# Kernel optimization log

Measured on AMD Instinct MI355X. Metric: run time of the kernel, lower is better.

## Reference

```python
import jax, jax.numpy as jnp
import numpy as np

N_TOKENS = 4096
N_EMBD = 1024
N_EXPERTS = 8
TOP_K = 2
TEMPERATURE = 1.0
PARAM_SCALE = 0.02


def setup_inputs() -> dict:
    key = jax.random.key(0)
    ks = jax.random.split(key, 6)
    x = jax.random.normal(ks[0], (N_TOKENS, N_EMBD), dtype=jnp.float32)
    gate_w = jax.random.normal(ks[1], (N_EMBD, N_EXPERTS), dtype=jnp.float32) * PARAM_SCALE
    w1 = jax.random.normal(ks[2], (N_EXPERTS, N_EMBD, 4 * N_EMBD), dtype=jnp.float32) * PARAM_SCALE
    b1 = jax.random.normal(ks[3], (N_EXPERTS, 4 * N_EMBD), dtype=jnp.float32) * PARAM_SCALE
    w2 = jax.random.normal(ks[4], (N_EXPERTS, 4 * N_EMBD, N_EMBD), dtype=jnp.float32) * PARAM_SCALE
    b2 = jax.random.normal(ks[5], (N_EXPERTS, N_EMBD), dtype=jnp.float32) * PARAM_SCALE
    return {"x": x, "gate_w": gate_w, "w1": w1, "b1": b1, "w2": w2, "b2": b2}


def reference(x, gate_w, w1, b1, w2, b2):
    # Gating: softmax with temperature, top-2, renormalize over the top-2.
    gate_logits = x @ gate_w                              # [N, E]
    gate_probs = jax.nn.softmax(gate_logits / TEMPERATURE, axis=-1)
    top_v, top_i = jax.lax.top_k(gate_probs, TOP_K)       # [N, k]
    top_v = top_v / jnp.sum(top_v, axis=-1, keepdims=True)
    # Per-expert combine weight: sum of renormalized top-k probs routed to e.
    one_hot = jax.nn.one_hot(top_i, N_EXPERTS, dtype=x.dtype)   # [N, k, E]
    combine = jnp.einsum('nk,nke->ne', top_v, one_hot)          # [N, E]
    # Dense expert evaluation (faithful math; loop over fixed small expert set).
    out = jnp.zeros_like(x)
    for e in range(N_EXPERTS):
        h = jax.nn.gelu(x @ w1[e] + b1[e], approximate=False)   # [N, 4C]
        y = h @ w2[e] + b2[e]                                   # [N, C]
        out = out + combine[:, e:e + 1] * y
    return out
```

## Files before the change

### kernel.cpp

```cpp
#include <hip/hip_runtime.h>
#include <math.h>

#define TOKENS 4096
#define EMBD   1024
#define HID    4096
#define NE     8
#define SLOTC  8320

typedef __attribute__((ext_vector_type(8))) short short8;
typedef __attribute__((ext_vector_type(4))) float f32x4;

#define GLOBAL_PTR(p) ((const __attribute__((address_space(1))) void*)(p))
#define LDS_PTR(p)    ((__attribute__((address_space(3))) void*)(p))

#define SWZ(row, q) ((row) * 32 + (((q) ^ (((row) >> 1) & 3)) * 8))

__device__ __forceinline__ unsigned short f2bf(float f) {
  unsigned int u = __float_as_uint(f);
  u += 0x7FFFu + ((u >> 16) & 1u);
  return (unsigned short)(u >> 16);
}
__device__ __forceinline__ float bf2f(unsigned short h) {
  return __uint_as_float((unsigned int)h << 16);
}

__device__ __forceinline__ float fast_gelu(float v) {
  float u = fabsf(v) * 0.70710678118654752f;
  float t = 1.0f / (1.0f + 0.3275911f * u);
  float poly = ((((1.061405429f * t - 1.453152027f) * t + 1.421413741f) * t
                 - 0.284496736f) * t + 0.254829592f) * t;
  float erf_abs = 1.0f - poly * __expf(-u * u);
  float er = (v < 0.0f) ? -erf_abs : erf_abs;
  return 0.5f * v * (1.0f + er);
}

__global__ __launch_bounds__(256) void k_gate_cvt(const float* __restrict__ x,
                                                  const float* __restrict__ gw,
                                                  unsigned short* __restrict__ xb,
                                                  int* __restrict__ idx2,
                                                  float* __restrict__ wv) {
  int wave = threadIdx.x >> 6, lane = threadIdx.x & 63;
  int t = blockIdx.x * 4 + wave;
  const float4* xr = (const float4*)(x + (size_t)t * EMBD);
  ushort4* xbr = (ushort4*)(xb + (size_t)t * EMBD);
  float acc[NE];
#pragma unroll
  for (int e = 0; e < NE; e++) acc[e] = 0.f;
#pragma unroll
  for (int ch = 0; ch < 4; ch++) {
    int i = ch * 64 + lane;
    float4 v = xr[i];
    ushort4 o;
    o.x = f2bf(v.x); o.y = f2bf(v.y); o.z = f2bf(v.z); o.w = f2bf(v.w);
    xbr[i] = o;
    int c = i * 4;
    const float* g0 = gw + (size_t)c * NE;
#pragma unroll
    for (int e = 0; e < NE; e++) acc[e] += v.x * g0[e];
#pragma unroll
    for (int e = 0; e < NE; e++) acc[e] += v.y * g0[NE + e];
#pragma unroll
    for (int e = 0; e < NE; e++) acc[e] += v.z * g0[2 * NE + e];
#pragma unroll
    for (int e = 0; e < NE; e++) acc[e] += v.w * g0[3 * NE + e];
  }
#pragma unroll
  for (int e = 0; e < NE; e++) {
#pragma unroll
    for (int off = 32; off > 0; off >>= 1) acc[e] += __shfl_down(acc[e], off);
  }
  if (lane == 0) {
    float best = -1e30f, second = -1e30f;
    int bi = 0, si = 0;
#pragma unroll
    for (int e = 0; e < NE; e++) {
      float l = acc[e];
      if (l > best) { second = best; si = bi; best = l; bi = e; }
      else if (l > second) { second = l; si = e; }
    }
    float b = expf(second - best);
    float w0 = 1.f / (1.f + b);
    float w1 = b / (1.f + b);
    idx2[2 * t] = bi; idx2[2 * t + 1] = si;
    wv[2 * t] = w0; wv[2 * t + 1] = w1;
  }
}

__global__ __launch_bounds__(256) void k_count(const int* __restrict__ idx2,
                                               int* __restrict__ ctrl) {
  __shared__ int cnt[NE];
  int tid = threadIdx.x;
  if (tid < NE) cnt[tid] = 0;
  __syncthreads();
  for (int i = tid; i < TOKENS * 2; i += 256) atomicAdd(&cnt[idx2[i]], 1);
  __syncthreads();
  if (tid == 0) {
    int off = 0;
#pragma unroll
    for (int e = 0; e < NE; e++) { int c = cnt[e]; ctrl[e] = c; ctrl[8 + e] = off; off += c; }
    ctrl[16] = off;
  }
  if (tid < NE) ctrl[17 + tid] = 0;
}

__global__ __launch_bounds__(256) void k_assign(const int* __restrict__ idx2,
                                                int* __restrict__ ctrl,
                                                int* __restrict__ token_list,
                                                int* __restrict__ tok2slot) {
  __shared__ int lpos[NE];
  __shared__ int lbase[NE];
  int tid = threadIdx.x;
  int t = blockIdx.x * 256 + tid;
  if (tid < NE) lpos[tid] = 0;
  __syncthreads();
  int e0 = idx2[2 * t], e1 = idx2[2 * t + 1];
  int p0 = atomicAdd(&lpos[e0], 1);
  int p1 = atomicAdd(&lpos[e1], 1);
  __syncthreads();
  if (tid < NE) lbase[tid] = atomicAdd(&ctrl[17 + tid], lpos[tid]);
  __syncthreads();
  int s0 = ctrl[8 + e0] + lbase[e0] + p0;
  int s1 = ctrl[8 + e1] + lbase[e1] + p1;
  token_list[s0] = t;
  token_list[s1] = t;
  tok2slot[2 * t] = s0;
  tok2slot[2 * t + 1] = s1;
}

__global__ __launch_bounds__(256) void k_trans(const float* __restrict__ in,
                                               unsigned short* __restrict__ out,
                                               int R, int C) {
  __shared__ unsigned short T[64 * 66];
  int e = blockIdx.z;
  const float* ine = in + (size_t)e * R * C;
  unsigned short* oute = out + (size_t)e * R * C;
  int r0 = blockIdx.y * 64;
  int c0 = blockIdx.x * 64;
  int tid = threadIdx.x;
  {
    int c4 = tid & 15;
    int rb = tid >> 4;
#pragma unroll
    for (int it = 0; it < 4; it++) {
      int r = rb + 16 * it;
      float4 v = *(const float4*)(ine + (size_t)(r0 + r) * C + c0 + 4 * c4);
      T[(4 * c4 + 0) * 66 + r] = f2bf(v.x);
      T[(4 * c4 + 1) * 66 + r] = f2bf(v.y);
      T[(4 * c4 + 2) * 66 + r] = f2bf(v.z);
      T[(4 * c4 + 3) * 66 + r] = f2bf(v.w);
    }
  }
  __syncthreads();
  {
    int rr = tid & 7;
    int cq = tid >> 3;
#pragma unroll
    for (int it = 0; it < 2; it++) {
      int c = cq + 32 * it;
      short8 o;
#pragma unroll
      for (int k = 0; k < 8; k++) o[k] = (short)T[c * 66 + 8 * rr + k];
      *(short8*)(oute + (size_t)(c0 + c) * R + r0 + 8 * rr) = o;
    }
  }
}

__global__ __launch_bounds__(256, 2) void k_gemm1(
    const unsigned short* __restrict__ xb,
    const unsigned short* __restrict__ w1t,
    const float* __restrict__ b1,
    const int* __restrict__ ctrl,
    const int* __restrict__ token_list,
    unsigned short* __restrict__ Hbuf) {
  int h = blockIdx.x;
  int e = h & 7;
  int j = h >> 3;
  int nb = (j & 31) * 128;
  int m_base = (j >> 5) * 128;
  int cnt = ctrl[e];
  if (m_base >= cnt) return;
  int off_e = ctrl[8 + e];
  int tid = threadIdx.x;
  int wave = tid >> 6, lane = tid & 63;

  __shared__ __align__(16) unsigned short As[2][128 * 32];
  __shared__ __align__(16) unsigned short Bs[2][128 * 32];

  int chS = (tid & 3) ^ ((tid >> 3) & 3);
  int rowA0 = tid >> 2;
  int rowA1 = 64 + (tid >> 2);
  int tok0 = token_list[off_e + min(m_base + rowA0, cnt - 1)];
  int tok1 = token_list[off_e + min(m_base + rowA1, cnt - 1)];
  const unsigned short* srcA0 = xb + (size_t)tok0 * EMBD + chS * 8;
  const unsigned short* srcA1 = xb + (size_t)tok1 * EMBD + chS * 8;
  const unsigned short* wb = w1t + (size_t)e * HID * EMBD;
  const unsigned short* srcB0 = wb + (size_t)(nb + rowA0) * EMBD + chS * 8;
  const unsigned short* srcB1 = wb + (size_t)(nb + rowA1) * EMBD + chS * 8;

  f32x4 acc[4][4];
#pragma unroll
  for (int i = 0; i < 4; i++)
#pragma unroll
    for (int j2 = 0; j2 < 4; j2++) acc[i][j2] = (f32x4){0.f, 0.f, 0.f, 0.f};

  int wm = (wave >> 1) * 64, wn = (wave & 1) * 64;
  int q4 = lane >> 4, cc = lane & 15;

#define STAGE1(buf, k0) do {                                                                            \
    __builtin_amdgcn_global_load_lds(GLOBAL_PTR(srcA0 + (k0)), LDS_PTR((char*)&As[buf][0] + wave * 1024), 16, 0, 0);        \
    __builtin_amdgcn_global_load_lds(GLOBAL_PTR(srcA1 + (k0)), LDS_PTR((char*)&As[buf][0] + 4096 + wave * 1024), 16, 0, 0); \
    __builtin_amdgcn_global_load_lds(GLOBAL_PTR(srcB0 + (k0)), LDS_PTR((char*)&Bs[buf][0] + wave * 1024), 16, 0, 0);        \
    __builtin_amdgcn_global_load_lds(GLOBAL_PTR(srcB1 + (k0)), LDS_PTR((char*)&Bs[buf][0] + 4096 + wave * 1024), 16, 0, 0); \
  } while (0)

#define COMPUTE1(buf) do {                                                                   \
    short8 af[4], bfr[4];                                                                    \
    _Pragma("unroll")                                                                        \
    for (int i = 0; i < 4; i++) af[i] = *(const short8*)(&As[buf][0] + SWZ(wm + i * 16 + cc, q4));   \
    _Pragma("unroll")                                                                        \
    for (int j2 = 0; j2 < 4; j2++) bfr[j2] = *(const short8*)(&Bs[buf][0] + SWZ(wn + j2 * 16 + cc, q4)); \
    _Pragma("unroll")                                                                        \
    for (int i = 0; i < 4; i++)                                                              \
      _Pragma("unroll")                                                                      \
      for (int j2 = 0; j2 < 4; j2++)                                                         \
        acc[i][j2] = __builtin_amdgcn_mfma_f32_16x16x32_bf16(af[i], bfr[j2], acc[i][j2], 0, 0, 0); \
  } while (0)

  STAGE1(0, 0);
  __syncthreads();
  int cur = 0;
  for (int k0 = 32; k0 < EMBD; k0 += 32) {
    STAGE1(cur ^ 1, k0);
    __builtin_amdgcn_sched_barrier(0);
    COMPUTE1(cur);
    __syncthreads();
    cur ^= 1;
  }
  COMPUTE1(cur);

  const float* b1e = b1 + (size_t)e * HID;
  float bias[4];
#pragma unroll
  for (int j2 = 0; j2 < 4; j2++) bias[j2] = b1e[nb + wn + j2 * 16 + cc];
#pragma unroll
  for (int i = 0; i < 4; i++) {
#pragma unroll
    for (int r = 0; r < 4; r++) {
      int m_loc = wm + i * 16 + q4 * 4 + r;
      int m = m_base + m_loc;
      if (m < cnt) {
        size_t hrow = (size_t)(off_e + m) * HID;
#pragma unroll
        for (int j2 = 0; j2 < 4; j2++)
          Hbuf[hrow + nb + wn + j2 * 16 + cc] = f2bf(fast_gelu(acc[i][j2][r] + bias[j2]));
      }
    }
  }
#undef STAGE1
#undef COMPUTE1
}

__global__ __launch_bounds__(256, 2) void k_gemm2(
    const unsigned short* __restrict__ Hbuf,
    const unsigned short* __restrict__ w2t,
    const int* __restrict__ ctrl,
    unsigned short* __restrict__ Yp) {
  int h = blockIdx.x;
  int e = h & 7;
  int s = (h >> 3) & 1;
  int rem = h >> 4;
  int m_base = (rem >> 3) * 128;
  int nb = (rem & 7) * 128;
  int cnt = ctrl[e];
  if (m_base >= cnt) return;
  int off_e = ctrl[8 + e];
  int tid = threadIdx.x;
  int wave = tid >> 6, lane = tid & 63;

  __shared__ __align__(16) unsigned short As[2][128 * 32];
  __shared__ __align__(16) unsigned short Bs[2][128 * 32];

  int chS = (tid & 3) ^ ((tid >> 3) & 3);
  int rowA0 = tid >> 2;
  int rowA1 = 64 + (tid >> 2);
  const unsigned short* srcA0 = Hbuf + (size_t)(off_e + m_base + rowA0) * HID + chS * 8;
  const unsigned short* srcA1 = Hbuf + (size_t)(off_e + m_base + rowA1) * HID + chS * 8;
  const unsigned short* wb = w2t + (size_t)e * EMBD * HID;
  const unsigned short* srcB0 = wb + (size_t)(nb + rowA0) * HID + chS * 8;
  const unsigned short* srcB1 = wb + (size_t)(nb + rowA1) * HID + chS * 8;

  f32x4 acc[4][4];
#pragma unroll
  for (int i = 0; i < 4; i++)
#pragma unroll
    for (int j2 = 0; j2 < 4; j2++) acc[i][j2] = (f32x4){0.f, 0.f, 0.f, 0.f};

  int wm = (wave >> 1) * 64, wn = (wave & 1) * 64;
  int q4 = lane >> 4, cc = lane & 15;

#define STAGE2(buf, k0) do {                                                                            \
    __builtin_amdgcn_global_load_lds(GLOBAL_PTR(srcA0 + (k0)), LDS_PTR((char*)&As[buf][0] + wave * 1024), 16, 0, 0);        \
    __builtin_amdgcn_global_load_lds(GLOBAL_PTR(srcA1 + (k0)), LDS_PTR((char*)&As[buf][0] + 4096 + wave * 1024), 16, 0, 0); \
    __builtin_amdgcn_global_load_lds(GLOBAL_PTR(srcB0 + (k0)), LDS_PTR((char*)&Bs[buf][0] + wave * 1024), 16, 0, 0);        \
    __builtin_amdgcn_global_load_lds(GLOBAL_PTR(srcB1 + (k0)), LDS_PTR((char*)&Bs[buf][0] + 4096 + wave * 1024), 16, 0, 0); \
  } while (0)

#define COMPUTE2(buf) do {                                                                   \
    short8 af[4], bfr[4];                                                                    \
    _Pragma("unroll")                                                                        \
    for (int i = 0; i < 4; i++) af[i] = *(const short8*)(&As[buf][0] + SWZ(wm + i * 16 + cc, q4));   \
    _Pragma("unroll")                                                                        \
    for (int j2 = 0; j2 < 4; j2++) bfr[j2] = *(const short8*)(&Bs[buf][0] + SWZ(wn + j2 * 16 + cc, q4)); \
    _Pragma("unroll")                                                                        \
    for (int i = 0; i < 4; i++)                                                              \
      _Pragma("unroll")                                                                      \
      for (int j2 = 0; j2 < 4; j2++)                                                         \
        acc[i][j2] = __builtin_amdgcn_mfma_f32_16x16x32_bf16(af[i], bfr[j2], acc[i][j2], 0, 0, 0); \
  } while (0)

  int kbeg = s * (HID / 2), kend = kbeg + HID / 2;
  STAGE2(0, kbeg);
  __syncthreads();
  int cur = 0;
  for (int k0 = kbeg + 32; k0 < kend; k0 += 32) {
    STAGE2(cur ^ 1, k0);
    __builtin_amdgcn_sched_barrier(0);
    COMPUTE2(cur);
    __syncthreads();
    cur ^= 1;
  }
  COMPUTE2(cur);

  unsigned short* Yps = Yp + (size_t)s * SLOTC * EMBD;
#pragma unroll
  for (int i = 0; i < 4; i++) {
#pragma unroll
    for (int r = 0; r < 4; r++) {
      int m_loc = wm + i * 16 + q4 * 4 + r;
      int m = m_base + m_loc;
      if (m < cnt) {
        size_t yrow = (size_t)(off_e + m) * EMBD;
#pragma unroll
        for (int j2 = 0; j2 < 4; j2++)
          Yps[yrow + nb + wn + j2 * 16 + cc] = f2bf(acc[i][j2][r]);
      }
    }
  }
#undef STAGE2
#undef COMPUTE2
}

__global__ __launch_bounds__(256) void k_combine(const unsigned short* __restrict__ Yp,
                                                 const float* __restrict__ b2,
                                                 const int* __restrict__ idx2,
                                                 const float* __restrict__ wv,
                                                 const int* __restrict__ tok2slot,
                                                 float* __restrict__ out) {
  int t = blockIdx.x;
  int tid = threadIdx.x;
  int c = tid * 4;
  int e0 = idx2[2 * t], e1 = idx2[2 * t + 1];
  float w0 = wv[2 * t], w1 = wv[2 * t + 1];
  int s0 = tok2slot[2 * t], s1 = tok2slot[2 * t + 1];
  ushort4 p00 = *(const ushort4*)(Yp + ((size_t)0 * SLOTC + s0) * EMBD + c);
  ushort4 p01 = *(const ushort4*)(Yp + ((size_t)1 * SLOTC + s0) * EMBD + c);
  ushort4 p10 = *(const ushort4*)(Yp + ((size_t)0 * SLOTC + s1) * EMBD + c);
  ushort4 p11 = *(const ushort4*)(Yp + ((size_t)1 * SLOTC + s1) * EMBD + c);
  float4 b20 = *(const float4*)(b2 + (size_t)e0 * EMBD + c);
  float4 b21 = *(const float4*)(b2 + (size_t)e1 * EMBD + c);
  float4 r;
  r.x = w0 * (bf2f(p00.x) + bf2f(p01.x) + b20.x) + w1 * (bf2f(p10.x) + bf2f(p11.x) + b21.x);
  r.y = w0 * (bf2f(p00.y) + bf2f(p01.y) + b20.y) + w1 * (bf2f(p10.y) + bf2f(p11.y) + b21.y);
  r.z = w0 * (bf2f(p00.z) + bf2f(p01.z) + b20.z) + w1 * (bf2f(p10.z) + bf2f(p11.z) + b21.z);
  r.w = w0 * (bf2f(p00.w) + bf2f(p01.w) + b20.w) + w1 * (bf2f(p10.w) + bf2f(p11.w) + b21.w);
  *(float4*)(out + (size_t)t * EMBD + c) = r;
}

extern "C" void kernel_launch(void* const* d_in, const int* in_sizes, int n_in,
                              void* d_out, int out_size, void* d_ws, size_t ws_size,
                              hipStream_t stream) {
  (void)in_sizes; (void)n_in; (void)out_size; (void)ws_size;
  const float* x      = (const float*)d_in[0];
  const float* gate_w = (const float*)d_in[1];
  const float* w1     = (const float*)d_in[2];
  const float* b1     = (const float*)d_in[3];
  const float* w2     = (const float*)d_in[4];
  const float* b2     = (const float*)d_in[5];
  float* out = (float*)d_out;

  char* ws = (char*)d_ws;
  size_t off = 0;
  auto alloc = [&](size_t bytes) {
    char* p = ws + off;
    off += (bytes + 255) & ~(size_t)255;
    return p;
  };
  unsigned short* xb    = (unsigned short*)alloc((size_t)TOKENS * EMBD * 2);
  unsigned short* w1t   = (unsigned short*)alloc((size_t)NE * HID * EMBD * 2);
  unsigned short* w2t   = (unsigned short*)alloc((size_t)NE * EMBD * HID * 2);
  unsigned short* Hbuf  = (unsigned short*)alloc((size_t)SLOTC * HID * 2);
  unsigned short* Yp    = (unsigned short*)alloc((size_t)2 * SLOTC * EMBD * 2);
  int*   token_list     = (int*)alloc((size_t)SLOTC * 4);
  int*   idx2           = (int*)alloc((size_t)TOKENS * 2 * 4);
  float* wv             = (float*)alloc((size_t)TOKENS * 2 * 4);
  int*   tok2slot       = (int*)alloc((size_t)TOKENS * 2 * 4);
  int*   ctrl           = (int*)alloc(32 * 4);

  k_gate_cvt<<<TOKENS / 4, 256, 0, stream>>>(x, gate_w, xb, idx2, wv);
  k_count<<<1, 256, 0, stream>>>(idx2, ctrl);
  k_assign<<<TOKENS / 256, 256, 0, stream>>>(idx2, ctrl, token_list, tok2slot);
  k_trans<<<dim3(HID / 64, EMBD / 64, NE), 256, 0, stream>>>(w1, w1t, EMBD, HID);
  k_trans<<<dim3(EMBD / 64, HID / 64, NE), 256, 0, stream>>>(w2, w2t, HID, EMBD);
  k_gemm1<<<8192, 256, 0, stream>>>(xb, w1t, b1, ctrl, token_list, Hbuf);
  k_gemm2<<<4096, 256, 0, stream>>>(Hbuf, w2t, ctrl, Yp);
  k_combine<<<TOKENS, 256, 0, stream>>>(Yp, b2, idx2, wv, tok2slot, out);
}
```

Baseline: 561.4 us.

## Use 256x256 tiles with 8 waves and 4-stage LDS pipeline in expert GEMMs

```diff
diff --git a/kernel.cpp b/kernel.cpp
--- a/kernel.cpp
+++ b/kernel.cpp
@@ -12,8 +12,6 @@
 
 #define GLOBAL_PTR(p) ((const __attribute__((address_space(1))) void*)(p))
 #define LDS_PTR(p)    ((__attribute__((address_space(3))) void*)(p))
-
-#define SWZ(row, q) ((row) * 32 + (((q) ^ (((row) >> 1) & 3)) * 8))
 
 __device__ __forceinline__ unsigned short f2bf(float f) {
   unsigned int u = __float_as_uint(f);
@@ -165,7 +163,32 @@
   }
 }
 
-__global__ __launch_bounds__(256, 2) void k_gemm1(
+
+#define STAGE_G(sA0_, sA1_, sB0_, sB1_, kk, sl) do {                                              \
+    __builtin_amdgcn_global_load_lds(GLOBAL_PTR((sA0_) + (kk)), LDS_PTR(lds + (sl) * 16384 + wave * 2048), 16, 0, 0);          \
+    __builtin_amdgcn_global_load_lds(GLOBAL_PTR((sA1_) + (kk)), LDS_PTR(lds + (sl) * 16384 + wave * 2048 + 1024), 16, 0, 0);   \
+    __builtin_amdgcn_global_load_lds(GLOBAL_PTR((sB0_) + (kk)), LDS_PTR(lds + 65536 + (sl) * 16384 + wave * 2048), 16, 0, 0);  \
+    __builtin_amdgcn_global_load_lds(GLOBAL_PTR((sB1_) + (kk)), LDS_PTR(lds + 65536 + (sl) * 16384 + wave * 2048 + 1024), 16, 0, 0); \
+  } while (0)
+
+#define STEP_BODY(sl) do {                                                                        \
+    const short8* Ap = (const short8*)(lds + (sl) * 16384 + aoff);                                \
+    const short8* Bp = (const short8*)(lds + 65536 + (sl) * 16384 + boff);                        \
+    short8 af[8], bfr[4];                                                                         \
+    _Pragma("unroll")                                                                             \
+    for (int f = 0; f < 8; f++) af[f] = Ap[f * 64];                                               \
+    _Pragma("unroll")                                                                             \
+    for (int n = 0; n < 4; n++) bfr[n] = Bp[n * 64];                                              \
+    __builtin_amdgcn_s_setprio(1);                                                                \
+    _Pragma("unroll")                                                                             \
+    for (int f = 0; f < 8; f++)                                                                   \
+      _Pragma("unroll")                                                                           \
+      for (int n = 0; n < 4; n++)                                                                 \
+        acc[f][n] = __builtin_amdgcn_mfma_f32_16x16x32_bf16(af[f], bfr[n], acc[f][n], 0, 0, 0);   \
+    __builtin_amdgcn_s_setprio(0);                                                                \
+  } while (0)
+
+__global__ __launch_bounds__(512, 2) void k_gemm1(
     const unsigned short* __restrict__ xb,
     const unsigned short* __restrict__ w1t,
     const float* __restrict__ b1,
@@ -175,92 +198,75 @@
   int h = blockIdx.x;
   int e = h & 7;
   int j = h >> 3;
-  int nb = (j & 31) * 128;
-  int m_base = (j >> 5) * 128;
+  int m_base = (j & 15) * 256;
+  int nb = (j >> 4) * 256;
   int cnt = ctrl[e];
   if (m_base >= cnt) return;
   int off_e = ctrl[8 + e];
   int tid = threadIdx.x;
   int wave = tid >> 6, lane = tid & 63;
-
-  __shared__ __align__(16) unsigned short As[2][128 * 32];
-  __shared__ __align__(16) unsigned short Bs[2][128 * 32];
-
-  int chS = (tid & 3) ^ ((tid >> 3) & 3);
-  int rowA0 = tid >> 2;
-  int rowA1 = 64 + (tid >> 2);
-  int tok0 = token_list[off_e + min(m_base + rowA0, cnt - 1)];
-  int tok1 = token_list[off_e + min(m_base + rowA1, cnt - 1)];
-  const unsigned short* srcA0 = xb + (size_t)tok0 * EMBD + chS * 8;
-  const unsigned short* srcA1 = xb + (size_t)tok1 * EMBD + chS * 8;
-  const unsigned short* wb = w1t + (size_t)e * HID * EMBD;
-  const unsigned short* srcB0 = wb + (size_t)(nb + rowA0) * EMBD + chS * 8;
-  const unsigned short* srcB1 = wb + (size_t)(nb + rowA1) * EMBD + chS * 8;
-
-  f32x4 acc[4][4];
-#pragma unroll
-  for (int i = 0; i < 4; i++)
-#pragma unroll
-    for (int j2 = 0; j2 < 4; j2++) acc[i][j2] = (f32x4){0.f, 0.f, 0.f, 0.f};
-
-  int wm = (wave >> 1) * 64, wn = (wave & 1) * 64;
+  int wr = wave >> 2, wc = wave & 3;
   int q4 = lane >> 4, cc = lane & 15;
 
-#define STAGE1(buf, k0) do {                                                                            \
-    __builtin_amdgcn_global_load_lds(GLOBAL_PTR(srcA0 + (k0)), LDS_PTR((char*)&As[buf][0] + wave * 1024), 16, 0, 0);        \
-    __builtin_amdgcn_global_load_lds(GLOBAL_PTR(srcA1 + (k0)), LDS_PTR((char*)&As[buf][0] + 4096 + wave * 1024), 16, 0, 0); \
-    __builtin_amdgcn_global_load_lds(GLOBAL_PTR(srcB0 + (k0)), LDS_PTR((char*)&Bs[buf][0] + wave * 1024), 16, 0, 0);        \
-    __builtin_amdgcn_global_load_lds(GLOBAL_PTR(srcB1 + (k0)), LDS_PTR((char*)&Bs[buf][0] + 4096 + wave * 1024), 16, 0, 0); \
-  } while (0)
-
-#define COMPUTE1(buf) do {                                                                   \
-    short8 af[4], bfr[4];                                                                    \
-    _Pragma("unroll")                                                                        \
-    for (int i = 0; i < 4; i++) af[i] = *(const short8*)(&As[buf][0] + SWZ(wm + i * 16 + cc, q4));   \
-    _Pragma("unroll")                                                                        \
-    for (int j2 = 0; j2 < 4; j2++) bfr[j2] = *(const short8*)(&Bs[buf][0] + SWZ(wn + j2 * 16 + cc, q4)); \
-    _Pragma("unroll")                                                                        \
-    for (int i = 0; i < 4; i++)                                                              \
-      _Pragma("unroll")                                                                      \
-      for (int j2 = 0; j2 < 4; j2++)                                                         \
-        acc[i][j2] = __builtin_amdgcn_mfma_f32_16x16x32_bf16(af[i], bfr[j2], acc[i][j2], 0, 0, 0); \
-  } while (0)
-
-  STAGE1(0, 0);
-  __syncthreads();
-  int cur = 0;
-  for (int k0 = 32; k0 < EMBD; k0 += 32) {
-    STAGE1(cur ^ 1, k0);
+  __shared__ __align__(16) char lds[131072];
+
+  int qg = (lane & 3) ^ ((lane >> 3) & 3);
+  int row0 = wave * 32 + (lane >> 2);
+  int row1 = row0 + 16;
+  int tok0 = token_list[off_e + min(m_base + row0, cnt - 1)];
+  int tok1 = token_list[off_e + min(m_base + row1, cnt - 1)];
+  const unsigned short* sA0 = xb + (size_t)tok0 * EMBD + qg * 8;
+  const unsigned short* sA1 = xb + (size_t)tok1 * EMBD + qg * 8;
+  const unsigned short* wbp = w1t + (size_t)e * HID * EMBD;
+  const unsigned short* sB0 = wbp + (size_t)(nb + row0) * EMBD + qg * 8;
+  const unsigned short* sB1 = wbp + (size_t)(nb + row1) * EMBD + qg * 8;
+
+  int swz = (q4 ^ ((cc >> 1) & 3)) * 16;
+  int aoff = (wr * 128 + cc) * 64 + swz;
+  int boff = (wc * 64 + cc) * 64 + swz;
+
+  f32x4 acc[8][4];
+#pragma unroll
+  for (int f = 0; f < 8; f++)
+#pragma unroll
+    for (int n = 0; n < 4; n++) acc[f][n] = (f32x4){0.f, 0.f, 0.f, 0.f};
+
+  STAGE_G(sA0, sA1, sB0, sB1, 0, 0);
+  STAGE_G(sA0, sA1, sB0, sB1, 32, 1);
+  STAGE_G(sA0, sA1, sB0, sB1, 64, 2);
+
+#pragma unroll 4
+  for (int c = 0; c < 32; ++c) {
+    asm volatile("s_waitcnt vmcnt(8)" ::: "memory");
+    __builtin_amdgcn_s_barrier();
     __builtin_amdgcn_sched_barrier(0);
-    COMPUTE1(cur);
-    __syncthreads();
-    cur ^= 1;
-  }
-  COMPUTE1(cur);
+    int kk = ((c + 3) * 32) & (EMBD - 1);
+    STAGE_G(sA0, sA1, sB0, sB1, kk, (c + 3) & 3);
+    STEP_BODY(c & 3);
+  }
+  asm volatile("s_waitcnt vmcnt(0)" ::: "memory");
 
   const float* b1e = b1 + (size_t)e * HID;
   float bias[4];
 #pragma unroll
-  for (int j2 = 0; j2 < 4; j2++) bias[j2] = b1e[nb + wn + j2 * 16 + cc];
-#pragma unroll
-  for (int i = 0; i < 4; i++) {
+  for (int n = 0; n < 4; n++) bias[n] = b1e[nb + wc * 64 + n * 16 + cc];
+#pragma unroll
+  for (int f = 0; f < 8; f++) {
 #pragma unroll
     for (int r = 0; r < 4; r++) {
-      int m_loc = wm + i * 16 + q4 * 4 + r;
+      int m_loc = wr * 128 + f * 16 + q4 * 4 + r;
       int m = m_base + m_loc;
       if (m < cnt) {
         size_t hrow = (size_t)(off_e + m) * HID;
 #pragma unroll
-        for (int j2 = 0; j2 < 4; j2++)
-          Hbuf[hrow + nb + wn + j2 * 16 + cc] = f2bf(fast_gelu(acc[i][j2][r] + bias[j2]));
+        for (int n = 0; n < 4; n++)
+          Hbuf[hrow + nb + wc * 64 + n * 16 + cc] = f2bf(fast_gelu(acc[f][n][r] + bias[n]));
       }
     }
   }
-#undef STAGE1
-#undef COMPUTE1
-}
-
-__global__ __launch_bounds__(256, 2) void k_gemm2(
+}
+
+__global__ __launch_bounds__(512, 2) void k_gemm2(
     const unsigned short* __restrict__ Hbuf,
     const unsigned short* __restrict__ w2t,
     const int* __restrict__ ctrl,
@@ -268,86 +274,71 @@
   int h = blockIdx.x;
   int e = h & 7;
   int s = (h >> 3) & 1;
-  int rem = h >> 4;
-  int m_base = (rem >> 3) * 128;
-  int nb = (rem & 7) * 128;
+  int j = h >> 4;
+  int m_base = (j & 15) * 256;
+  int nb = (j >> 4) * 256;
   int cnt = ctrl[e];
   if (m_base >= cnt) return;
   int off_e = ctrl[8 + e];
   int tid = threadIdx.x;
   int wave = tid >> 6, lane = tid & 63;
-
-  __shared__ __align__(16) unsigned short As[2][128 * 32];
-  __shared__ __align__(16) unsigned short Bs[2][128 * 32];
-
-  int chS = (tid & 3) ^ ((tid >> 3) & 3);
-  int rowA0 = tid >> 2;
-  int rowA1 = 64 + (tid >> 2);
-  const unsigned short* srcA0 = Hbuf + (size_t)(off_e + m_base + rowA0) * HID + chS * 8;
-  const unsigned short* srcA1 = Hbuf + (size_t)(off_e + m_base + rowA1) * HID + chS * 8;
-  const unsigned short* wb = w2t + (size_t)e * EMBD * HID;
-  const unsigned short* srcB0 = wb + (size_t)(nb + rowA0) * HID + chS * 8;
-  const unsigned short* srcB1 = wb + (size_t)(nb + rowA1) * HID + chS * 8;
-
-  f32x4 acc[4][4];
-#pragma unroll
-  for (int i = 0; i < 4; i++)
-#pragma unroll
-    for (int j2 = 0; j2 < 4; j2++) acc[i][j2] = (f32x4){0.f, 0.f, 0.f, 0.f};
-
-  int wm = (wave >> 1) * 64, wn = (wave & 1) * 64;
+  int wr = wave >> 2, wc = wave & 3;
   int q4 = lane >> 4, cc = lane & 15;
 
-#define STAGE2(buf, k0) do {                                                                            \
-    __builtin_amdgcn_global_load_lds(GLOBAL_PTR(srcA0 + (k0)), LDS_PTR((char*)&As[buf][0] + wave * 1024), 16, 0, 0);        \
-    __builtin_amdgcn_global_load_lds(GLOBAL_PTR(srcA1 + (k0)), LDS_PTR((char*)&As[buf][0] + 4096 + wave * 1024), 16, 0, 0); \
-    __builtin_amdgcn_global_load_lds(GLOBAL_PTR(srcB0 + (k0)), LDS_PTR((char*)&Bs[buf][0] + wave * 1024), 16, 0, 0);        \
-    __builtin_amdgcn_global_load_lds(GLOBAL_PTR(srcB1 + (k0)), LDS_PTR((char*)&Bs[buf][0] + 4096 + wave * 1024), 16, 0, 0); \
-  } while (0)
-
-#define COMPUTE2(buf) do {                                                                   \
-    short8 af[4], bfr[4];                                                                    \
-    _Pragma("unroll")                                                                        \
-    for (int i = 0; i < 4; i++) af[i] = *(const short8*)(&As[buf][0] + SWZ(wm + i * 16 + cc, q4));   \
-    _Pragma("unroll")                                                                        \
-    for (int j2 = 0; j2 < 4; j2++) bfr[j2] = *(const short8*)(&Bs[buf][0] + SWZ(wn + j2 * 16 + cc, q4)); \
-    _Pragma("unroll")                                                                        \
-    for (int i = 0; i < 4; i++)                                                              \
-      _Pragma("unroll")                                                                      \
-      for (int j2 = 0; j2 < 4; j2++)                                                         \
-        acc[i][j2] = __builtin_amdgcn_mfma_f32_16x16x32_bf16(af[i], bfr[j2], acc[i][j2], 0, 0, 0); \
-  } while (0)
-
-  int kbeg = s * (HID / 2), kend = kbeg + HID / 2;
-  STAGE2(0, kbeg);
-  __syncthreads();
-  int cur = 0;
-  for (int k0 = kbeg + 32; k0 < kend; k0 += 32) {
-    STAGE2(cur ^ 1, k0);
+  __shared__ __align__(16) char lds[131072];
+
+  int qg = (lane & 3) ^ ((lane >> 3) & 3);
+  int row0 = wave * 32 + (lane >> 2);
+  int row1 = row0 + 16;
+  int ar0 = off_e + min(m_base + row0, cnt - 1);
+  int ar1 = off_e + min(m_base + row1, cnt - 1);
+  int kbeg = s * (HID / 2);
+  const unsigned short* sA0 = Hbuf + (size_t)ar0 * HID + kbeg + qg * 8;
+  const unsigned short* sA1 = Hbuf + (size_t)ar1 * HID + kbeg + qg * 8;
+  const unsigned short* wbp = w2t + (size_t)e * EMBD * HID;
+  const unsigned short* sB0 = wbp + (size_t)(nb + row0) * HID + kbeg + qg * 8;
+  const unsigned short* sB1 = wbp + (size_t)(nb + row1) * HID + kbeg + qg * 8;
+
+  int swz = (q4 ^ ((cc >> 1) & 3)) * 16;
+  int aoff = (wr * 128 + cc) * 64 + swz;
+  int boff = (wc * 64 + cc) * 64 + swz;
+
+  f32x4 acc[8][4];
+#pragma unroll
+  for (int f = 0; f < 8; f++)
+#pragma unroll
+    for (int n = 0; n < 4; n++) acc[f][n] = (f32x4){0.f, 0.f, 0.f, 0.f};
+
+  STAGE_G(sA0, sA1, sB0, sB1, 0, 0);
+  STAGE_G(sA0, sA1, sB0, sB1, 32, 1);
+  STAGE_G(sA0, sA1, sB0, sB1, 64, 2);
+
+#pragma unroll 4
+  for (int c = 0; c < 64; ++c) {
+    asm volatile("s_waitcnt vmcnt(8)" ::: "memory");
+    __builtin_amdgcn_s_barrier();
     __builtin_amdgcn_sched_barrier(0);
-    COMPUTE2(cur);
-    __syncthreads();
-    cur ^= 1;
-  }
-  COMPUTE2(cur);
+    int kk = ((c + 3) * 32) & (HID / 2 - 1);
+    STAGE_G(sA0, sA1, sB0, sB1, kk, (c + 3) & 3);
+    STEP_BODY(c & 3);
+  }
+  asm volatile("s_waitcnt vmcnt(0)" ::: "memory");
 
   unsigned short* Yps = Yp + (size_t)s * SLOTC * EMBD;
 #pragma unroll
-  for (int i = 0; i < 4; i++) {
+  for (int f = 0; f < 8; f++) {
 #pragma unroll
     for (int r = 0; r < 4; r++) {
-      int m_loc = wm + i * 16 + q4 * 4 + r;
+      int m_loc = wr * 128 + f * 16 + q4 * 4 + r;
       int m = m_base + m_loc;
       if (m < cnt) {
         size_t yrow = (size_t)(off_e + m) * EMBD;
 #pragma unroll
-        for (int j2 = 0; j2 < 4; j2++)
-          Yps[yrow + nb + wn + j2 * 16 + cc] = f2bf(acc[i][j2][r]);
+        for (int n = 0; n < 4; n++)
+          Yps[yrow + nb + wc * 64 + n * 16 + cc] = f2bf(acc[f][n][r]);
       }
     }
   }
-#undef STAGE2
-#undef COMPUTE2
 }
 
 __global__ __launch_bounds__(256) void k_combine(const unsigned short* __restrict__ Yp,
@@ -411,7 +402,7 @@
   k_assign<<<TOKENS / 256, 256, 0, stream>>>(idx2, ctrl, token_list, tok2slot);
   k_trans<<<dim3(HID / 64, EMBD / 64, NE), 256, 0, stream>>>(w1, w1t, EMBD, HID);
   k_trans<<<dim3(EMBD / 64, HID / 64, NE), 256, 0, stream>>>(w2, w2t, HID, EMBD);
-  k_gemm1<<<8192, 256, 0, stream>>>(xb, w1t, b1, ctrl, token_list, Hbuf);
-  k_gemm2<<<4096, 256, 0, stream>>>(Hbuf, w2t, ctrl, Yp);
+  k_gemm1<<<2048, 512, 0, stream>>>(xb, w1t, b1, ctrl, token_list, Hbuf);
+  k_gemm2<<<1024, 512, 0, stream>>>(Hbuf, w2t, ctrl, Yp);
   k_combine<<<TOKENS, 256, 0, stream>>>(Yp, b2, idx2, wv, tok2slot, out);
 }
```

Result: slower. 601.7 us (+7.2%).

## Triple-buffer GEMM K-loops with vmcnt waits and M-fastest block order

Applied to the files above, without the earlier changes.

```diff
diff --git a/kernel.cpp b/kernel.cpp
--- a/kernel.cpp
+++ b/kernel.cpp
@@ -12,8 +12,6 @@
 
 #define GLOBAL_PTR(p) ((const __attribute__((address_space(1))) void*)(p))
 #define LDS_PTR(p)    ((__attribute__((address_space(3))) void*)(p))
-
-#define SWZ(row, q) ((row) * 32 + (((q) ^ (((row) >> 1) & 3)) * 8))
 
 __device__ __forceinline__ unsigned short f2bf(float f) {
   unsigned int u = __float_as_uint(f);
@@ -165,7 +163,45 @@
   }
 }
 
-__global__ __launch_bounds__(256, 2) void k_gemm1(
+
+#define SB __builtin_amdgcn_sched_barrier(0)
+#define VM4 asm volatile("s_waitcnt vmcnt(4)" ::: "memory")
+#define VM0 asm volatile("s_waitcnt vmcnt(0)" ::: "memory")
+
+#define STAGE_T(sl, koff) do {                                                                                   \
+    __builtin_amdgcn_global_load_lds(GLOBAL_PTR(sA0 + (koff)), LDS_PTR(lds + (sl) * 16384 + wave * 1024), 16, 0, 0);          \
+    __builtin_amdgcn_global_load_lds(GLOBAL_PTR(sA1 + (koff)), LDS_PTR(lds + (sl) * 16384 + 4096 + wave * 1024), 16, 0, 0);   \
+    __builtin_amdgcn_global_load_lds(GLOBAL_PTR(sB0 + (koff)), LDS_PTR(lds + (sl) * 16384 + 8192 + wave * 1024), 16, 0, 0);   \
+    __builtin_amdgcn_global_load_lds(GLOBAL_PTR(sB1 + (koff)), LDS_PTR(lds + (sl) * 16384 + 12288 + wave * 1024), 16, 0, 0);  \
+  } while (0)
+
+#define KLOOP(NT) do {                                                                            \
+    int sl = 0, sl2 = 2;                                                                          \
+    for (int kt = 0; kt < (NT); ++kt) {                                                           \
+      if (kt < (NT) - 1) { VM4; } else { VM0; }                                                   \
+      SB;                                                                                         \
+      __builtin_amdgcn_s_barrier();                                                               \
+      SB;                                                                                         \
+      if (kt + 2 < (NT)) STAGE_T(sl2, (kt + 2) * 32);                                             \
+      SB;                                                                                         \
+      const char* Ab_ = lds + sl * 16384;                                                         \
+      const char* Bb_ = Ab_ + 8192;                                                               \
+      short8 af[4], bg[4];                                                                        \
+      _Pragma("unroll")                                                                           \
+      for (int i = 0; i < 4; i++) af[i] = *(const short8*)(Ab_ + aoff + i * 1024);                \
+      _Pragma("unroll")                                                                           \
+      for (int n = 0; n < 4; n++) bg[n] = *(const short8*)(Bb_ + boff + n * 1024);                \
+      _Pragma("unroll")                                                                           \
+      for (int i = 0; i < 4; i++)                                                                 \
+        _Pragma("unroll")                                                                         \
+        for (int n = 0; n < 4; n++)                                                               \
+          acc[i][n] = __builtin_amdgcn_mfma_f32_16x16x32_bf16(af[i], bg[n], acc[i][n], 0, 0, 0);  \
+      sl = (sl == 2) ? 0 : sl + 1;                                                                \
+      sl2 = (sl2 == 2) ? 0 : sl2 + 1;                                                             \
+    }                                                                                             \
+  } while (0)
+
+__global__ __launch_bounds__(256, 3) void k_gemm1(
     const unsigned short* __restrict__ xb,
     const unsigned short* __restrict__ w1t,
     const float* __restrict__ b1,
@@ -175,73 +211,47 @@
   int h = blockIdx.x;
   int e = h & 7;
   int j = h >> 3;
-  int nb = (j & 31) * 128;
-  int m_base = (j >> 5) * 128;
+  int m_base = (j & 31) * 128;
+  int nb = (j >> 5) * 128;
   int cnt = ctrl[e];
   if (m_base >= cnt) return;
   int off_e = ctrl[8 + e];
   int tid = threadIdx.x;
   int wave = tid >> 6, lane = tid & 63;
 
-  __shared__ __align__(16) unsigned short As[2][128 * 32];
-  __shared__ __align__(16) unsigned short Bs[2][128 * 32];
-
-  int chS = (tid & 3) ^ ((tid >> 3) & 3);
+  __shared__ __align__(16) char lds[49152];
+
+  int chS = (lane & 3) ^ ((lane >> 3) & 3);
   int rowA0 = tid >> 2;
-  int rowA1 = 64 + (tid >> 2);
+  int rowA1 = 64 + rowA0;
   int tok0 = token_list[off_e + min(m_base + rowA0, cnt - 1)];
   int tok1 = token_list[off_e + min(m_base + rowA1, cnt - 1)];
-  const unsigned short* srcA0 = xb + (size_t)tok0 * EMBD + chS * 8;
-  const unsigned short* srcA1 = xb + (size_t)tok1 * EMBD + chS * 8;
-  const unsigned short* wb = w1t + (size_t)e * HID * EMBD;
-  const unsigned short* srcB0 = wb + (size_t)(nb + rowA0) * EMBD + chS * 8;
-  const unsigned short* srcB1 = wb + (size_t)(nb + rowA1) * EMBD + chS * 8;
-
-  f32x4 acc[4][4];
-#pragma unroll
-  for (int i = 0; i < 4; i++)
-#pragma unroll
-    for (int j2 = 0; j2 < 4; j2++) acc[i][j2] = (f32x4){0.f, 0.f, 0.f, 0.f};
+  const unsigned short* sA0 = xb + (size_t)tok0 * EMBD + chS * 8;
+  const unsigned short* sA1 = xb + (size_t)tok1 * EMBD + chS * 8;
+  const unsigned short* wbp = w1t + (size_t)e * HID * EMBD;
+  const unsigned short* sB0 = wbp + (size_t)(nb + rowA0) * EMBD + chS * 8;
+  const unsigned short* sB1 = wbp + (size_t)(nb + rowA1) * EMBD + chS * 8;
 
   int wm = (wave >> 1) * 64, wn = (wave & 1) * 64;
   int q4 = lane >> 4, cc = lane & 15;
-
-#define STAGE1(buf, k0) do {                                                                            \
-    __builtin_amdgcn_global_load_lds(GLOBAL_PTR(srcA0 + (k0)), LDS_PTR((char*)&As[buf][0] + wave * 1024), 16, 0, 0);        \
-    __builtin_amdgcn_global_load_lds(GLOBAL_PTR(srcA1 + (k0)), LDS_PTR((char*)&As[buf][0] + 4096 + wave * 1024), 16, 0, 0); \
-    __builtin_amdgcn_global_load_lds(GLOBAL_PTR(srcB0 + (k0)), LDS_PTR((char*)&Bs[buf][0] + wave * 1024), 16, 0, 0);        \
-    __builtin_amdgcn_global_load_lds(GLOBAL_PTR(srcB1 + (k0)), LDS_PTR((char*)&Bs[buf][0] + 4096 + wave * 1024), 16, 0, 0); \
-  } while (0)
-
-#define COMPUTE1(buf) do {                                                                   \
-    short8 af[4], bfr[4];                                                                    \
-    _Pragma("unroll")                                                                        \
-    for (int i = 0; i < 4; i++) af[i] = *(const short8*)(&As[buf][0] + SWZ(wm + i * 16 + cc, q4));   \
-    _Pragma("unroll")                                                                        \
-    for (int j2 = 0; j2 < 4; j2++) bfr[j2] = *(const short8*)(&Bs[buf][0] + SWZ(wn + j2 * 16 + cc, q4)); \
-    _Pragma("unroll")                                                                        \
-    for (int i = 0; i < 4; i++)                                                              \
-      _Pragma("unroll")                                                                      \
-      for (int j2 = 0; j2 < 4; j2++)                                                         \
-        acc[i][j2] = __builtin_amdgcn_mfma_f32_16x16x32_bf16(af[i], bfr[j2], acc[i][j2], 0, 0, 0); \
-  } while (0)
-
-  STAGE1(0, 0);
-  __syncthreads();
-  int cur = 0;
-  for (int k0 = 32; k0 < EMBD; k0 += 32) {
-    STAGE1(cur ^ 1, k0);
-    __builtin_amdgcn_sched_barrier(0);
-    COMPUTE1(cur);
-    __syncthreads();
-    cur ^= 1;
-  }
-  COMPUTE1(cur);
+  int swz = (q4 ^ ((cc >> 1) & 3)) * 16;
+  int aoff = (wm + cc) * 64 + swz;
+  int boff = (wn + cc) * 64 + swz;
+
+  f32x4 acc[4][4];
+#pragma unroll
+  for (int i = 0; i < 4; i++)
+#pragma unroll
+    for (int n = 0; n < 4; n++) acc[i][n] = (f32x4){0.f, 0.f, 0.f, 0.f};
+
+  STAGE_T(0, 0);
+  STAGE_T(1, 32);
+  KLOOP(32);
 
   const float* b1e = b1 + (size_t)e * HID;
   float bias[4];
 #pragma unroll
-  for (int j2 = 0; j2 < 4; j2++) bias[j2] = b1e[nb + wn + j2 * 16 + cc];
+  for (int n = 0; n < 4; n++) bias[n] = b1e[nb + wn + n * 16 + cc];
 #pragma unroll
   for (int i = 0; i < 4; i++) {
 #pragma unroll
@@ -251,16 +261,14 @@
       if (m < cnt) {
         size_t hrow = (size_t)(off_e + m) * HID;
 #pragma unroll
-        for (int j2 = 0; j2 < 4; j2++)
-          Hbuf[hrow + nb + wn + j2 * 16 + cc] = f2bf(fast_gelu(acc[i][j2][r] + bias[j2]));
+        for (int n = 0; n < 4; n++)
+          Hbuf[hrow + nb + wn + n * 16 + cc] = f2bf(fast_gelu(acc[i][n][r] + bias[n]));
       }
     }
   }
-#undef STAGE1
-#undef COMPUTE1
-}
-
-__global__ __launch_bounds__(256, 2) void k_gemm2(
+}
+
+__global__ __launch_bounds__(256, 3) void k_gemm2(
     const unsigned short* __restrict__ Hbuf,
     const unsigned short* __restrict__ w2t,
     const int* __restrict__ ctrl,
@@ -269,67 +277,43 @@
   int e = h & 7;
   int s = (h >> 3) & 1;
   int rem = h >> 4;
-  int m_base = (rem >> 3) * 128;
-  int nb = (rem & 7) * 128;
+  int m_base = (rem & 31) * 128;
+  int nb = (rem >> 5) * 128;
   int cnt = ctrl[e];
   if (m_base >= cnt) return;
   int off_e = ctrl[8 + e];
   int tid = threadIdx.x;
   int wave = tid >> 6, lane = tid & 63;
 
-  __shared__ __align__(16) unsigned short As[2][128 * 32];
-  __shared__ __align__(16) unsigned short Bs[2][128 * 32];
-
-  int chS = (tid & 3) ^ ((tid >> 3) & 3);
+  __shared__ __align__(16) char lds[49152];
+
+  int chS = (lane & 3) ^ ((lane >> 3) & 3);
   int rowA0 = tid >> 2;
-  int rowA1 = 64 + (tid >> 2);
-  const unsigned short* srcA0 = Hbuf + (size_t)(off_e + m_base + rowA0) * HID + chS * 8;
-  const unsigned short* srcA1 = Hbuf + (size_t)(off_e + m_base + rowA1) * HID + chS * 8;
-  const unsigned short* wb = w2t + (size_t)e * EMBD * HID;
-  const unsigned short* srcB0 = wb + (size_t)(nb + rowA0) * HID + chS * 8;
-  const unsigned short* srcB1 = wb + (size_t)(nb + rowA1) * HID + chS * 8;
-
-  f32x4 acc[4][4];
-#pragma unroll
-  for (int i = 0; i < 4; i++)
-#pragma unroll
-    for (int j2 = 0; j2 < 4; j2++) acc[i][j2] = (f32x4){0.f, 0.f, 0.f, 0.f};
+  int rowA1 = 64 + rowA0;
+  int ar0 = off_e + min(m_base + rowA0, cnt - 1);
+  int ar1 = off_e + min(m_base + rowA1, cnt - 1);
+  int kbeg = s * (HID / 2);
+  const unsigned short* sA0 = Hbuf + (size_t)ar0 * HID + kbeg + chS * 8;
+  const unsigned short* sA1 = Hbuf + (size_t)ar1 * HID + kbeg + chS * 8;
+  const unsigned short* wbp = w2t + (size_t)e * EMBD * HID;
+  const unsigned short* sB0 = wbp + (size_t)(nb + rowA0) * HID + kbeg + chS * 8;
+  const unsigned short* sB1 = wbp + (size_t)(nb + rowA1) * HID + kbeg + chS * 8;
 
   int wm = (wave >> 1) * 64, wn = (wave & 1) * 64;
   int q4 = lane >> 4, cc = lane & 15;
-
-#define STAGE2(buf, k0) do {                                                                            \
-    __builtin_amdgcn_global_load_lds(GLOBAL_PTR(srcA0 + (k0)), LDS_PTR((char*)&As[buf][0] + wave * 1024), 16, 0, 0);        \
-    __builtin_amdgcn_global_load_lds(GLOBAL_PTR(srcA1 + (k0)), LDS_PTR((char*)&As[buf][0] + 4096 + wave * 1024), 16, 0, 0); \
-    __builtin_amdgcn_global_load_lds(GLOBAL_PTR(srcB0 + (k0)), LDS_PTR((char*)&Bs[buf][0] + wave * 1024), 16, 0, 0);        \
-    __builtin_amdgcn_global_load_lds(GLOBAL_PTR(srcB1 + (k0)), LDS_PTR((char*)&Bs[buf][0] + 4096 + wave * 1024), 16, 0, 0); \
-  } while (0)
-
-#define COMPUTE2(buf) do {                                                                   \
-    short8 af[4], bfr[4];                                                                    \
-    _Pragma("unroll")                                                                        \
-    for (int i = 0; i < 4; i++) af[i] = *(const short8*)(&As[buf][0] + SWZ(wm + i * 16 + cc, q4));   \
-    _Pragma("unroll")                                                                        \
-    for (int j2 = 0; j2 < 4; j2++) bfr[j2] = *(const short8*)(&Bs[buf][0] + SWZ(wn + j2 * 16 + cc, q4)); \
-    _Pragma("unroll")                                                                        \
-    for (int i = 0; i < 4; i++)                                                              \
-      _Pragma("unroll")                                                                      \
-      for (int j2 = 0; j2 < 4; j2++)                                                         \
-        acc[i][j2] = __builtin_amdgcn_mfma_f32_16x16x32_bf16(af[i], bfr[j2], acc[i][j2], 0, 0, 0); \
-  } while (0)
-
-  int kbeg = s * (HID / 2), kend = kbeg + HID / 2;
-  STAGE2(0, kbeg);
-  __syncthreads();
-  int cur = 0;
-  for (int k0 = kbeg + 32; k0 < kend; k0 += 32) {
-    STAGE2(cur ^ 1, k0);
-    __builtin_amdgcn_sched_barrier(0);
-    COMPUTE2(cur);
-    __syncthreads();
-    cur ^= 1;
-  }
-  COMPUTE2(cur);
+  int swz = (q4 ^ ((cc >> 1) & 3)) * 16;
+  int aoff = (wm + cc) * 64 + swz;
+  int boff = (wn + cc) * 64 + swz;
+
+  f32x4 acc[4][4];
+#pragma unroll
+  for (int i = 0; i < 4; i++)
+#pragma unroll
+    for (int n = 0; n < 4; n++) acc[i][n] = (f32x4){0.f, 0.f, 0.f, 0.f};
+
+  STAGE_T(0, 0);
+  STAGE_T(1, 32);
+  KLOOP(64);
 
   unsigned short* Yps = Yp + (size_t)s * SLOTC * EMBD;
 #pragma unroll
@@ -341,13 +325,11 @@
       if (m < cnt) {
         size_t yrow = (size_t)(off_e + m) * EMBD;
 #pragma unroll
-        for (int j2 = 0; j2 < 4; j2++)
-          Yps[yrow + nb + wn + j2 * 16 + cc] = f2bf(acc[i][j2][r]);
+        for (int n = 0; n < 4; n++)
+          Yps[yrow + nb + wn + n * 16 + cc] = f2bf(acc[i][n][r]);
       }
     }
   }
-#undef STAGE2
-#undef COMPUTE2
 }
 
 __global__ __launch_bounds__(256) void k_combine(const unsigned short* __restrict__ Yp,
```

After: 566.0 us. No clear change (+0.8%).
